# Optimization experiments

Hardware: AMD Instinct MI355X
Metric: run time of the kernel (lower is better)

## Reference

```python
import jax, jax.numpy as jnp
import numpy as np

N_NODES = 100000
N_EDGES = 1600000
D_IN = 128
D_HID = 128
D_OUT = 64


def _glorot(key, shape):
    lim = float(np.sqrt(6.0 / (shape[0] + shape[1])))
    return jax.random.uniform(key, shape, jnp.float32, -lim, lim)


def setup_inputs() -> dict:
    key = jax.random.key(0)
    ks = jax.random.split(key, 8)
    x = jax.random.normal(ks[0], (N_NODES, D_IN), jnp.float32)
    edge_index = jax.random.randint(ks[1], (2, N_EDGES), 0, N_NODES, jnp.int64)
    # SAGEConv layer 0: in=128 -> out=128 (lin_l with bias on aggregated, lin_r no bias on root)
    W_l0 = _glorot(ks[2], (D_IN, D_HID))
    b_l0 = jnp.zeros((D_HID,), jnp.float32)
    W_r0 = _glorot(ks[3], (D_IN, D_HID))
    # SAGEConv layer 1: in=128 -> out=64
    W_l1 = _glorot(ks[4], (D_HID, D_OUT))
    b_l1 = jnp.zeros((D_OUT,), jnp.float32)
    W_r1 = _glorot(ks[5], (D_HID, D_OUT))
    return {"x": x, "edge_index": edge_index,
            "W_l0": W_l0, "b_l0": b_l0, "W_r0": W_r0,
            "W_l1": W_l1, "b_l1": b_l1, "W_r1": W_r1}


def _sage_conv(x, src, dst, W_l, b_l, W_r):
    # mean aggregation of source features at targets (PyG SAGEConv default aggr='mean')
    msgs = x[src]                                              # [E, d_in] irregular gather
    agg = jax.ops.segment_sum(msgs, dst, num_segments=N_NODES)  # [N, d_in]
    cnt = jax.ops.segment_sum(jnp.ones((src.shape[0],), x.dtype), dst,
                              num_segments=N_NODES)            # [N]
    mean = agg / jnp.maximum(cnt, 1.0)[:, None]
    return mean @ W_l + b_l + x @ W_r


def reference(x, edge_index, W_l0, b_l0, W_r0, W_l1, b_l1, W_r1):
    src, dst = edge_index[0], edge_index[1]
    h = _sage_conv(x, src, dst, W_l0, b_l0, W_r0)
    h = jax.nn.relu(h)
    # dropout is identity at inference (training=False)
    out = _sage_conv(h, src, dst, W_l1, b_l1, W_r1)
    return out
```

## Files before the change

### kernel.cpp

```cpp
#include <hip/hip_runtime.h>
#include <type_traits>

#define NN 100000
#define NE 1600000
#define DF 128
#define NBKT 196
#define BKT_SHIFT 9
#define EPB 6250
#define NPB2 391

typedef unsigned short ushort_t;
typedef unsigned int uint_t;
typedef __bf16 bf16x8 __attribute__((ext_vector_type(8)));
typedef float f32x4 __attribute__((ext_vector_type(4)));

union ABFrag { uint4 u; bf16x8 v; ushort_t s[8]; };

__device__ __forceinline__ ushort_t f2bf(float f) {
    uint_t u;
    __builtin_memcpy(&u, &f, 4);
    uint_t rounding = 0x7FFFu + ((u >> 16) & 1u);
    u += rounding;
    return (ushort_t)(u >> 16);
}
__device__ __forceinline__ float lo_f(uint_t u) { return __uint_as_float(u << 16); }
__device__ __forceinline__ float hi_f(uint_t u) { return __uint_as_float(u & 0xffff0000u); }
__device__ __forceinline__ uint_t pack2(float a, float b) {
    return (uint_t)f2bf(a) | ((uint_t)f2bf(b) << 16);
}

__device__ __forceinline__ int detect64(const int* ei, int* s64) {
    if (threadIdx.x < 64) {
        int v = ei[threadIdx.x];
        bool ok = ((threadIdx.x & 1) == 0) || (v == 0);
        unsigned long long m = __ballot(ok);
        if (threadIdx.x == 0) *s64 = (m == 0xFFFFFFFFFFFFFFFFULL) ? 1 : 0;
    }
    __syncthreads();
    return *s64;
}

__global__ __launch_bounds__(256) void k_bktcnt(const int* __restrict__ ei,
                                                int* __restrict__ M) {
    __shared__ int cnt[NBKT];
    __shared__ int s64;
    int t = threadIdx.x, blk = blockIdx.x;
    int is64 = detect64(ei, &s64);
    for (int i = t; i < NBKT; i += 256) cnt[i] = 0;
    __syncthreads();
    int e0 = blk * EPB;
    if (is64) {
        const long long* p = (const long long*)ei;
        for (int i = t; i < EPB; i += 256) {
            int d = (int)p[(size_t)NE + e0 + i];
            atomicAdd(&cnt[d >> BKT_SHIFT], 1);
        }
    } else {
        for (int i = t; i < EPB; i += 256) {
            int d = ei[NE + e0 + i];
            atomicAdd(&cnt[d >> BKT_SHIFT], 1);
        }
    }
    __syncthreads();
    for (int i = t; i < NBKT; i += 256) M[i * 256 + blk] = cnt[i];
}

__global__ __launch_bounds__(256) void k_colscan(int* __restrict__ M, int* __restrict__ colsum) {
    __shared__ int sm[256];
    int t = threadIdx.x, b = blockIdx.x;
    int v = M[b * 256 + t];
    sm[t] = v;
    __syncthreads();
    for (int o = 1; o < 256; o <<= 1) {
        int add = (t >= o) ? sm[t - o] : 0;
        __syncthreads();
        sm[t] += add;
        __syncthreads();
    }
    M[b * 256 + t] = sm[t] - v;
    if (t == 255) colsum[b] = sm[255];
}

__global__ __launch_bounds__(256) void k_bktscan(const int* __restrict__ colsum,
                                                 int* __restrict__ bkbase, int* __restrict__ rs) {
    __shared__ int sm[256];
    int t = threadIdx.x;
    int v = (t < NBKT) ? colsum[t] : 0;
    sm[t] = v;
    __syncthreads();
    for (int o = 1; o < 256; o <<= 1) {
        int add = (t >= o) ? sm[t - o] : 0;
        __syncthreads();
        sm[t] += add;
        __syncthreads();
    }
    if (t <= NBKT) bkbase[t] = sm[t] - v;
    if (t == 0) rs[NN] = NE;
}

__global__ void k_scan512(const int* __restrict__ c2, int* __restrict__ dbase) {
    __shared__ int sm[512];
    int t = threadIdx.x;
    int v = c2[t];
    sm[t] = v;
    __syncthreads();
    for (int o = 1; o < 512; o <<= 1) {
        int add = (t >= o) ? sm[t - o] : 0;
        __syncthreads();
        sm[t] += add;
        __syncthreads();
    }
    dbase[t] = sm[t] - v;
}

__global__ __launch_bounds__(256) void k_bktscatter(const int* __restrict__ ei,
                                                    const int* __restrict__ M,
                                                    const int* __restrict__ bkbase,
                                                    uint2* __restrict__ tmp) {
    __shared__ int cur[NBKT];
    __shared__ int s64;
    int t = threadIdx.x, blk = blockIdx.x;
    int is64 = detect64(ei, &s64);
    for (int i = t; i < NBKT; i += 256) cur[i] = bkbase[i] + M[i * 256 + blk];
    __syncthreads();
    int e0 = blk * EPB;
    if (is64) {
        const long long* p = (const long long*)ei;
        for (int i = t; i < EPB; i += 256) {
            int e = e0 + i;
            int s = (int)p[e], d = (int)p[(size_t)NE + e];
            int pos = atomicAdd(&cur[d >> BKT_SHIFT], 1);
            tmp[pos] = make_uint2((uint_t)s, (uint_t)d);
        }
    } else {
        for (int i = t; i < EPB; i += 256) {
            int e = e0 + i;
            int s = ei[e], d = ei[NE + e];
            int pos = atomicAdd(&cur[d >> BKT_SHIFT], 1);
            tmp[pos] = make_uint2((uint_t)s, (uint_t)d);
        }
    }
}

__global__ __launch_bounds__(256) void k_bktsort(const uint2* __restrict__ tmp,
                                                 const int* __restrict__ bkbase,
                                                 int* __restrict__ rs, int* __restrict__ esrc) {
    __shared__ int hist[512];
    __shared__ int curp[512];
    int t = threadIdx.x, b = blockIdx.x;
    int nbase = b << BKT_SHIFT;
    int bb = bkbase[b], be = bkbase[b + 1];
    hist[t] = 0;
    hist[t + 256] = 0;
    __syncthreads();
    for (int i = bb + t; i < be; i += 256)
        atomicAdd(&hist[(int)tmp[i].y - nbase], 1);
    __syncthreads();
    int ov0 = hist[t], ov1 = hist[t + 256];
    for (int o = 1; o < 512; o <<= 1) {
        int v0 = (t >= o) ? hist[t - o] : 0;
        int v1 = (t + 256 >= o) ? hist[t + 256 - o] : 0;
        __syncthreads();
        hist[t] += v0;
        hist[t + 256] += v1;
        __syncthreads();
    }
    int ex0 = bb + hist[t] - ov0;
    int ex1 = bb + hist[t + 256] - ov1;
    int n0 = nbase + t, n1 = nbase + t + 256;
    if (n0 < NN) rs[n0] = ex0;
    if (n1 < NN) rs[n1] = ex1;
    curp[t] = ex0;
    curp[t + 256] = ex1;
    __syncthreads();
    for (int i = bb + t; i < be; i += 256) {
        uint2 pr = tmp[i];
        int pos = atomicAdd(&curp[(int)pr.y - nbase], 1);
        esrc[pos] = (int)pr.x;
    }
}

__global__ __launch_bounds__(256) void k_dcnt(const int* __restrict__ rs, int* __restrict__ M2) {
    __shared__ int cnt[512];
    int t = threadIdx.x, b = blockIdx.x;
    cnt[t] = 0;
    cnt[t + 256] = 0;
    __syncthreads();
    int base = b * NPB2;
    for (int i = t; i < NPB2; i += 256) {
        int n = base + i;
        if (n < NN) {
            int d = rs[n + 1] - rs[n];
            if (d > 511) d = 511;
            atomicAdd(&cnt[d], 1);
        }
    }
    __syncthreads();
    M2[t * 256 + b] = cnt[t];
    M2[(t + 256) * 256 + b] = cnt[t + 256];
}

__global__ __launch_bounds__(256) void k_dperm(const int* __restrict__ rs,
                                               const int* __restrict__ M2,
                                               const int* __restrict__ dbase,
                                               int* __restrict__ perm) {
    __shared__ int cur[512];
    int t = threadIdx.x, b = blockIdx.x;
    cur[t] = dbase[t] + M2[t * 256 + b];
    cur[t + 256] = dbase[t + 256] + M2[(t + 256) * 256 + b];
    __syncthreads();
    int base = b * NPB2;
    for (int i = t; i < NPB2; i += 256) {
        int n = base + i;
        if (n < NN) {
            int d = rs[n + 1] - rs[n];
            if (d > 511) d = 511;
            int pos = atomicAdd(&cur[d], 1);
            perm[pos] = n;
        }
    }
}

#define CAST_B 12501
__global__ void k_prep(const float* __restrict__ x, ushort_t* __restrict__ xb,
                       const float* __restrict__ Wl0, const float* __restrict__ Wr0,
                       ushort_t* __restrict__ pw0,
                       const float* __restrict__ Wl1, const float* __restrict__ Wr1,
                       ushort_t* __restrict__ pw1) {
    const int n4 = NN * DF / 4;
    int blk = blockIdx.x, t = threadIdx.x;
    if (blk < CAST_B) {
        int i = blk * 256 + t;
        if (i < n4) {
            float4 f = ((const float4*)x)[i];
            uint2 o;
            o.x = pack2(f.x, f.y);
            o.y = pack2(f.z, f.w);
            ((uint2*)xb)[i] = o;
        } else if (i < n4 + 32) {
            ((uint2*)xb)[i] = make_uint2(0u, 0u);
        }
    } else if (blk < CAST_B + 128) {
        int idx = (blk - CAST_B) * 256 + t;
        int j = idx & 7;
        int lane = (idx >> 3) & 63;
        int rem = idx / 512;
        int tt = rem % 8;
        int s = rem / 8;
        int quad = lane >> 4, l16 = lane & 15;
        int k = (s & 3) * 32 + quad * 8 + j;
        int n = tt * 16 + l16;
        const float* W = (s < 4) ? Wl0 : Wr0;
        pw0[idx] = f2bf(W[k * 128 + n]);
    } else {
        int idx = (blk - CAST_B - 128) * 256 + t;
        int j = idx & 7;
        int lane = (idx >> 3) & 63;
        int rem = idx / 512;
        int tt = rem % 8;
        int s = rem / 8;
        int quad = lane >> 4, l16 = lane & 15;
        int k = s * 32 + quad * 8 + j;
        int n = (tt & 3) * 16 + l16;
        const float* W = (tt < 4) ? Wl1 : Wr1;
        pw1[idx] = f2bf(W[k * 64 + n]);
    }
}

__global__ __launch_bounds__(256) void k_agg0(const ushort_t* __restrict__ xb,
                                              const int* __restrict__ rs,
                                              const int* __restrict__ esrc,
                                              const int* __restrict__ perm,
                                              ushort_t* __restrict__ outm) {
    int wv = threadIdx.x >> 6;
    int lane = threadIdx.x & 63;
    int l16 = lane & 15, quad = lane >> 4, gbase = lane & 48;
    int slot = (blockIdx.x * 4 + wv) * 4 + quad;
    int n = perm[slot];
    int s0 = rs[n];
    int deg = rs[n + 1] - s0;
    if (deg == 0) s0 = 0;
    int md = deg;
    md = max(md, __shfl_xor(md, 16));
    md = max(md, __shfl_xor(md, 32));
    float acc[8] = {0.f, 0.f, 0.f, 0.f, 0.f, 0.f, 0.f, 0.f};
    const ushort_t* fb = xb + l16 * 8;
    int clampIdx = (deg > 0) ? deg - 1 : 0;
    for (int c = 0; c < md; c += 16) {
        int ii = c + l16;
        if (ii > clampIdx) ii = clampIdx;
        int my = esrc[s0 + ii];
        uint4 v[16];
#pragma unroll
        for (int e = 0; e < 16; e++) {
            int r = __shfl(my, gbase + e);
            r = (c + e < deg) ? r : NN;
            v[e] = *(const uint4*)(fb + (size_t)r * DF);
        }
#pragma unroll
        for (int e = 0; e < 16; e++) {
            acc[0] += lo_f(v[e].x); acc[1] += hi_f(v[e].x);
            acc[2] += lo_f(v[e].y); acc[3] += hi_f(v[e].y);
            acc[4] += lo_f(v[e].z); acc[5] += hi_f(v[e].z);
            acc[6] += lo_f(v[e].w); acc[7] += hi_f(v[e].w);
        }
    }
    float inv = 1.0f / (float)(deg > 0 ? deg : 1);
    uint4 o;
    o.x = pack2(acc[0] * inv, acc[1] * inv);
    o.y = pack2(acc[2] * inv, acc[3] * inv);
    o.z = pack2(acc[4] * inv, acc[5] * inv);
    o.w = pack2(acc[6] * inv, acc[7] * inv);
    *(uint4*)(outm + (size_t)n * DF + l16 * 8) = o;
}

__global__ __launch_bounds__(256) void k_gemm0(const ushort_t* __restrict__ A0,
                                               const ushort_t* __restrict__ A1,
                                               const ushort_t* __restrict__ Wpk,
                                               const float* __restrict__ bias,
                                               ushort_t* __restrict__ out) {
    int warp = threadIdx.x >> 6;
    int lane = threadIdx.x & 63;
    int quad = lane >> 4;
    int l16 = lane & 15;
    int m0 = blockIdx.x * 64 + warp * 16;

    int rowA = m0 + l16;
    if (rowA >= NN) rowA = NN - 1;
    const int kofs = quad * 8;

    f32x4 acc[8];
#pragma unroll
    for (int t = 0; t < 8; t++) acc[t] = (f32x4){0.f, 0.f, 0.f, 0.f};

#pragma unroll
    for (int s = 0; s < 8; s++) {
        const ushort_t* Ab = (s < 4) ? A0 : A1;
        int kk = (s & 3) * 32 + kofs;
        ABFrag a;
        a.u = *(const uint4*)(Ab + (size_t)rowA * DF + kk);
#pragma unroll
        for (int t = 0; t < 8; t++) {
            ABFrag b;
            b.u = *(const uint4*)(Wpk + ((size_t)(s * 8 + t) * 64 + lane) * 8);
            acc[t] = __builtin_amdgcn_mfma_f32_16x16x32_bf16(a.v, b.v, acc[t], 0, 0, 0);
        }
    }

#pragma unroll
    for (int t = 0; t < 8; t++) {
        int col = t * 16 + l16;
        float bv = bias[col];
#pragma unroll
        for (int r = 0; r < 4; r++) {
            int row = m0 + quad * 4 + r;
            if (row < NN) {
                float v = fmaxf(acc[t][r] + bv, 0.f);
                out[(size_t)row * DF + col] = f2bf(v);
            }
        }
    }
}

__global__ __launch_bounds__(256) void k_gemm2(const ushort_t* __restrict__ A,
                                               const ushort_t* __restrict__ Wpk,
                                               const float* __restrict__ bias,
                                               ushort_t* __restrict__ tbuf,
                                               float* __restrict__ rbuf) {
    int warp = threadIdx.x >> 6;
    int lane = threadIdx.x & 63;
    int quad = lane >> 4;
    int l16 = lane & 15;
    int m0 = blockIdx.x * 64 + warp * 16;

    int rowA = m0 + l16;
    if (rowA >= NN) rowA = NN - 1;
    const int kofs = quad * 8;

    f32x4 acc[8];
#pragma unroll
    for (int t = 0; t < 8; t++) acc[t] = (f32x4){0.f, 0.f, 0.f, 0.f};

#pragma unroll
    for (int s = 0; s < 4; s++) {
        int kk = s * 32 + kofs;
        ABFrag a;
        a.u = *(const uint4*)(A + (size_t)rowA * DF + kk);
#pragma unroll
        for (int t = 0; t < 8; t++) {
            ABFrag b;
            b.u = *(const uint4*)(Wpk + ((size_t)(s * 8 + t) * 64 + lane) * 8);
            acc[t] = __builtin_amdgcn_mfma_f32_16x16x32_bf16(a.v, b.v, acc[t], 0, 0, 0);
        }
    }

#pragma unroll
    for (int t = 0; t < 8; t++) {
        int cc = (t & 3) * 16 + l16;
        if (t < 4) {
#pragma unroll
            for (int r = 0; r < 4; r++) {
                int row = m0 + quad * 4 + r;
                if (row < NN) tbuf[(size_t)row * 64 + cc] = f2bf(acc[t][r]);
            }
        } else {
            float bv = bias[cc];
#pragma unroll
            for (int r = 0; r < 4; r++) {
                int row = m0 + quad * 4 + r;
                if (row < NN) rbuf[(size_t)row * 64 + cc] = acc[t][r] + bv;
            }
        }
    }
    if (blockIdx.x == 0 && threadIdx.x < 32)
        ((uint_t*)(tbuf + (size_t)NN * 64))[threadIdx.x] = 0u;
}

__global__ __launch_bounds__(256) void k_agg2(const ushort_t* __restrict__ tbuf,
                                              const float* __restrict__ rbuf,
                                              const int* __restrict__ rs,
                                              const int* __restrict__ esrc,
                                              const int* __restrict__ perm,
                                              float* __restrict__ out) {
    int wv = threadIdx.x >> 6;
    int lane = threadIdx.x & 63;
    int li = lane & 7;
    int gbase = lane & 56;
    int slot = (blockIdx.x * 4 + wv) * 8 + (lane >> 3);
    int n = perm[slot];
    int s0 = rs[n];
    int deg = rs[n + 1] - s0;
    if (deg == 0) s0 = 0;
    int md = deg;
    md = max(md, __shfl_xor(md, 8));
    md = max(md, __shfl_xor(md, 16));
    md = max(md, __shfl_xor(md, 32));
    float acc[8] = {0.f, 0.f, 0.f, 0.f, 0.f, 0.f, 0.f, 0.f};
    const ushort_t* fb = tbuf + li * 8;
    int clampIdx = (deg > 0) ? deg - 1 : 0;
    for (int c = 0; c < md; c += 8) {
        int ii = c + li;
        if (ii > clampIdx) ii = clampIdx;
        int my = esrc[s0 + ii];
        uint4 v[8];
#pragma unroll
        for (int e = 0; e < 8; e++) {
            int r = __shfl(my, gbase + e);
            r = (c + e < deg) ? r : NN;
            v[e] = *(const uint4*)(fb + (size_t)r * 64);
        }
#pragma unroll
        for (int e = 0; e < 8; e++) {
            acc[0] += lo_f(v[e].x); acc[1] += hi_f(v[e].x);
            acc[2] += lo_f(v[e].y); acc[3] += hi_f(v[e].y);
            acc[4] += lo_f(v[e].z); acc[5] += hi_f(v[e].z);
            acc[6] += lo_f(v[e].w); acc[7] += hi_f(v[e].w);
        }
    }
    float inv = 1.0f / (float)(deg > 0 ? deg : 1);
    const float4* rp = (const float4*)(rbuf + (size_t)n * 64 + li * 8);
    float4 ra = rp[0], rb = rp[1];
    float4 oa, ob;
    oa.x = acc[0] * inv + ra.x; oa.y = acc[1] * inv + ra.y;
    oa.z = acc[2] * inv + ra.z; oa.w = acc[3] * inv + ra.w;
    ob.x = acc[4] * inv + rb.x; ob.y = acc[5] * inv + rb.y;
    ob.z = acc[6] * inv + rb.z; ob.w = acc[7] * inv + rb.w;
    float4* op = (float4*)(out + (size_t)n * 64 + li * 8);
    op[0] = oa;
    op[1] = ob;
}

extern "C" void kernel_launch(void* const* d_in, const int* in_sizes, int n_in,
                              void* d_out, int out_size, void* d_ws, size_t ws_size,
                              hipStream_t stream) {
    const float* x   = (const float*)d_in[0];
    const int*   ei  = (const int*)d_in[1];
    const float* Wl0 = (const float*)d_in[2];
    const float* bl0 = (const float*)d_in[3];
    const float* Wr0 = (const float*)d_in[4];
    const float* Wl1 = (const float*)d_in[5];
    const float* bl1 = (const float*)d_in[6];
    const float* Wr1 = (const float*)d_in[7];
    float* out = (float*)d_out;

    char* ws = (char*)d_ws;
    size_t off = 0;
    auto alloc = [&](size_t b) {
        size_t o = off;
        off += (b + 255) & ~(size_t)255;
        return o;
    };
    int* rs      = (int*)(ws + alloc((size_t)(NN + 1) * 4));
    int* M       = (int*)(ws + alloc((size_t)NBKT * 256 * 4));
    int* colsum  = (int*)(ws + alloc((size_t)NBKT * 4));
    int* bkbase  = (int*)(ws + alloc((size_t)(NBKT + 1) * 4));
    int* M2      = (int*)(ws + alloc((size_t)512 * 256 * 4));
    int* colsum2 = (int*)(ws + alloc((size_t)512 * 4));
    int* dbase   = (int*)(ws + alloc((size_t)512 * 4));
    int* perm    = (int*)(ws + alloc((size_t)NN * 4));
    int* esrc    = (int*)(ws + alloc((size_t)NE * 4));
    ushort_t* pw0  = (ushort_t*)(ws + alloc((size_t)8 * 8 * 512 * 2));
    ushort_t* pw1  = (ushort_t*)(ws + alloc((size_t)4 * 8 * 512 * 2));
    ushort_t* xb   = (ushort_t*)(ws + alloc((size_t)(NN + 1) * DF * 2));
    ushort_t* mean = (ushort_t*)(ws + alloc((size_t)NN * DF * 2));
    ushort_t* h    = (ushort_t*)(ws + alloc((size_t)NN * DF * 2));
    ushort_t* tbuf = (ushort_t*)(ws + alloc((size_t)(NN + 1) * 64 * 2));
    uint2* tmp = (uint2*)mean;
    float* rbuf = (float*)mean;

    k_bktcnt<<<256, 256, 0, stream>>>(ei, M);
    k_colscan<<<NBKT, 256, 0, stream>>>(M, colsum);
    k_bktscan<<<1, 256, 0, stream>>>(colsum, bkbase, rs);
    k_bktscatter<<<256, 256, 0, stream>>>(ei, M, bkbase, tmp);
    k_bktsort<<<NBKT, 256, 0, stream>>>(tmp, bkbase, rs, esrc);
    k_dcnt<<<256, 256, 0, stream>>>(rs, M2);
    k_colscan<<<512, 256, 0, stream>>>(M2, colsum2);
    k_scan512<<<1, 512, 0, stream>>>(colsum2, dbase);
    k_dperm<<<256, 256, 0, stream>>>(rs, M2, dbase, perm);
    k_prep<<<CAST_B + 128 + 64, 256, 0, stream>>>(x, xb, Wl0, Wr0, pw0, Wl1, Wr1, pw1);

    k_agg0<<<NN / 16, 256, 0, stream>>>(xb, rs, esrc, perm, mean);
    k_gemm0<<<(NN + 63) / 64, 256, 0, stream>>>(mean, xb, pw0, bl0, h);
    k_gemm2<<<(NN + 63) / 64, 256, 0, stream>>>(h, pw1, bl1, tbuf, rbuf);
    k_agg2<<<NN / 32, 256, 0, stream>>>(tbuf, rbuf, rs, esrc, perm, out);
}
```

Before: 339.0 us.

## Fuse the two GEMMs through LDS and bound gather loops by group max degree

The layer-0 GEMM and the layer-1 projection GEMM become one kernel. The ReLU'd hidden tile is staged in shared memory, so h is no longer written to or read back from global memory, and one launch is removed. rbuf gets its own buffer because mean is still being read while rbuf is written. Both aggregation kernels now loop only up to the group's max degree, in chunks of 4 with a scalar tail, instead of always issuing 16 or 8 gathers. In exchange, fewer loads are in flight per iteration, and the fused kernel uses LDS and a barrier.

```diff
diff --git a/kernel.cpp b/kernel.cpp
--- a/kernel.cpp
+++ b/kernel.cpp
@@ -274,8 +274,8 @@
                                               ushort_t* __restrict__ outm) {
     int wv = threadIdx.x >> 6;
     int lane = threadIdx.x & 63;
-    int l16 = lane & 15, quad = lane >> 4, gbase = lane & 48;
-    int slot = (blockIdx.x * 4 + wv) * 4 + quad;
+    int l16 = lane & 15, gbase = lane & 48;
+    int slot = (blockIdx.x * 4 + wv) * 4 + (lane >> 4);
     int n = perm[slot];
     int s0 = rs[n];
     int deg = rs[n + 1] - s0;
@@ -290,19 +290,37 @@
         int ii = c + l16;
         if (ii > clampIdx) ii = clampIdx;
         int my = esrc[s0 + ii];
-        uint4 v[16];
-#pragma unroll
-        for (int e = 0; e < 16; e++) {
+        int lim = md - c;
+        if (lim > 16) lim = 16;
+        int e = 0;
+        for (; e + 4 <= lim; e += 4) {
+            int r0 = __shfl(my, gbase + e);
+            int r1 = __shfl(my, gbase + e + 1);
+            int r2 = __shfl(my, gbase + e + 2);
+            int r3 = __shfl(my, gbase + e + 3);
+            r0 = (c + e < deg) ? r0 : NN;
+            r1 = (c + e + 1 < deg) ? r1 : NN;
+            r2 = (c + e + 2 < deg) ? r2 : NN;
+            r3 = (c + e + 3 < deg) ? r3 : NN;
+            uint4 v0 = *(const uint4*)(fb + (size_t)r0 * DF);
+            uint4 v1 = *(const uint4*)(fb + (size_t)r1 * DF);
+            uint4 v2 = *(const uint4*)(fb + (size_t)r2 * DF);
+            uint4 v3 = *(const uint4*)(fb + (size_t)r3 * DF);
+            acc[0] += lo_f(v0.x); acc[1] += hi_f(v0.x); acc[2] += lo_f(v0.y); acc[3] += hi_f(v0.y);
+            acc[4] += lo_f(v0.z); acc[5] += hi_f(v0.z); acc[6] += lo_f(v0.w); acc[7] += hi_f(v0.w);
+            acc[0] += lo_f(v1.x); acc[1] += hi_f(v1.x); acc[2] += lo_f(v1.y); acc[3] += hi_f(v1.y);
+            acc[4] += lo_f(v1.z); acc[5] += hi_f(v1.z); acc[6] += lo_f(v1.w); acc[7] += hi_f(v1.w);
+            acc[0] += lo_f(v2.x); acc[1] += hi_f(v2.x); acc[2] += lo_f(v2.y); acc[3] += hi_f(v2.y);
+            acc[4] += lo_f(v2.z); acc[5] += hi_f(v2.z); acc[6] += lo_f(v2.w); acc[7] += hi_f(v2.w);
+            acc[0] += lo_f(v3.x); acc[1] += hi_f(v3.x); acc[2] += lo_f(v3.y); acc[3] += hi_f(v3.y);
+            acc[4] += lo_f(v3.z); acc[5] += hi_f(v3.z); acc[6] += lo_f(v3.w); acc[7] += hi_f(v3.w);
+        }
+        for (; e < lim; ++e) {
             int r = __shfl(my, gbase + e);
             r = (c + e < deg) ? r : NN;
-            v[e] = *(const uint4*)(fb + (size_t)r * DF);
-        }
-#pragma unroll
-        for (int e = 0; e < 16; e++) {
-            acc[0] += lo_f(v[e].x); acc[1] += hi_f(v[e].x);
-            acc[2] += lo_f(v[e].y); acc[3] += hi_f(v[e].y);
-            acc[4] += lo_f(v[e].z); acc[5] += hi_f(v[e].z);
-            acc[6] += lo_f(v[e].w); acc[7] += hi_f(v[e].w);
+            uint4 v = *(const uint4*)(fb + (size_t)r * DF);
+            acc[0] += lo_f(v.x); acc[1] += hi_f(v.x); acc[2] += lo_f(v.y); acc[3] += hi_f(v.y);
+            acc[4] += lo_f(v.z); acc[5] += hi_f(v.z); acc[6] += lo_f(v.w); acc[7] += hi_f(v.w);
         }
     }
     float inv = 1.0f / (float)(deg > 0 ? deg : 1);
@@ -314,11 +332,15 @@
     *(uint4*)(outm + (size_t)n * DF + l16 * 8) = o;
 }
 
-__global__ __launch_bounds__(256) void k_gemm0(const ushort_t* __restrict__ A0,
+__global__ __launch_bounds__(256) void k_gemmF(const ushort_t* __restrict__ A0,
                                                const ushort_t* __restrict__ A1,
-                                               const ushort_t* __restrict__ Wpk,
-                                               const float* __restrict__ bias,
-                                               ushort_t* __restrict__ out) {
+                                               const ushort_t* __restrict__ pw0,
+                                               const float* __restrict__ bl0,
+                                               const ushort_t* __restrict__ pw1,
+                                               const float* __restrict__ bl1,
+                                               ushort_t* __restrict__ tbuf,
+                                               float* __restrict__ rbuf) {
+    __shared__ ushort_t h_lds[64][136];
     int warp = threadIdx.x >> 6;
     int lane = threadIdx.x & 63;
     int quad = lane >> 4;
@@ -342,58 +364,34 @@
 #pragma unroll
         for (int t = 0; t < 8; t++) {
             ABFrag b;
-            b.u = *(const uint4*)(Wpk + ((size_t)(s * 8 + t) * 64 + lane) * 8);
+            b.u = *(const uint4*)(pw0 + ((size_t)(s * 8 + t) * 64 + lane) * 8);
             acc[t] = __builtin_amdgcn_mfma_f32_16x16x32_bf16(a.v, b.v, acc[t], 0, 0, 0);
         }
     }
-
 #pragma unroll
     for (int t = 0; t < 8; t++) {
         int col = t * 16 + l16;
-        float bv = bias[col];
-#pragma unroll
-        for (int r = 0; r < 4; r++) {
-            int row = m0 + quad * 4 + r;
-            if (row < NN) {
-                float v = fmaxf(acc[t][r] + bv, 0.f);
-                out[(size_t)row * DF + col] = f2bf(v);
-            }
-        }
-    }
-}
-
-__global__ __launch_bounds__(256) void k_gemm2(const ushort_t* __restrict__ A,
-                                               const ushort_t* __restrict__ Wpk,
-                                               const float* __restrict__ bias,
-                                               ushort_t* __restrict__ tbuf,
-                                               float* __restrict__ rbuf) {
-    int warp = threadIdx.x >> 6;
-    int lane = threadIdx.x & 63;
-    int quad = lane >> 4;
-    int l16 = lane & 15;
-    int m0 = blockIdx.x * 64 + warp * 16;
-
-    int rowA = m0 + l16;
-    if (rowA >= NN) rowA = NN - 1;
-    const int kofs = quad * 8;
-
-    f32x4 acc[8];
-#pragma unroll
-    for (int t = 0; t < 8; t++) acc[t] = (f32x4){0.f, 0.f, 0.f, 0.f};
-
+        float bv = bl0[col];
+#pragma unroll
+        for (int r = 0; r < 4; r++)
+            h_lds[warp * 16 + quad * 4 + r][col] = f2bf(fmaxf(acc[t][r] + bv, 0.f));
+    }
+    __syncthreads();
+
+    f32x4 c1[8];
+#pragma unroll
+    for (int t = 0; t < 8; t++) c1[t] = (f32x4){0.f, 0.f, 0.f, 0.f};
 #pragma unroll
     for (int s = 0; s < 4; s++) {
-        int kk = s * 32 + kofs;
         ABFrag a;
-        a.u = *(const uint4*)(A + (size_t)rowA * DF + kk);
+        a.u = *(const uint4*)&h_lds[warp * 16 + l16][s * 32 + kofs];
 #pragma unroll
         for (int t = 0; t < 8; t++) {
             ABFrag b;
-            b.u = *(const uint4*)(Wpk + ((size_t)(s * 8 + t) * 64 + lane) * 8);
-            acc[t] = __builtin_amdgcn_mfma_f32_16x16x32_bf16(a.v, b.v, acc[t], 0, 0, 0);
-        }
-    }
-
+            b.u = *(const uint4*)(pw1 + ((size_t)(s * 8 + t) * 64 + lane) * 8);
+            c1[t] = __builtin_amdgcn_mfma_f32_16x16x32_bf16(a.v, b.v, c1[t], 0, 0, 0);
+        }
+    }
 #pragma unroll
     for (int t = 0; t < 8; t++) {
         int cc = (t & 3) * 16 + l16;
@@ -401,14 +399,14 @@
 #pragma unroll
             for (int r = 0; r < 4; r++) {
                 int row = m0 + quad * 4 + r;
-                if (row < NN) tbuf[(size_t)row * 64 + cc] = f2bf(acc[t][r]);
+                if (row < NN) tbuf[(size_t)row * 64 + cc] = f2bf(c1[t][r]);
             }
         } else {
-            float bv = bias[cc];
+            float bv = bl1[cc];
 #pragma unroll
             for (int r = 0; r < 4; r++) {
                 int row = m0 + quad * 4 + r;
-                if (row < NN) rbuf[(size_t)row * 64 + cc] = acc[t][r] + bv;
+                if (row < NN) rbuf[(size_t)row * 64 + cc] = c1[t][r] + bv;
             }
         }
     }
@@ -442,19 +440,37 @@
         int ii = c + li;
         if (ii > clampIdx) ii = clampIdx;
         int my = esrc[s0 + ii];
-        uint4 v[8];
-#pragma unroll
-        for (int e = 0; e < 8; e++) {
+        int lim = md - c;
+        if (lim > 8) lim = 8;
+        int e = 0;
+        for (; e + 4 <= lim; e += 4) {
+            int r0 = __shfl(my, gbase + e);
+            int r1 = __shfl(my, gbase + e + 1);
+            int r2 = __shfl(my, gbase + e + 2);
+            int r3 = __shfl(my, gbase + e + 3);
+            r0 = (c + e < deg) ? r0 : NN;
+            r1 = (c + e + 1 < deg) ? r1 : NN;
+            r2 = (c + e + 2 < deg) ? r2 : NN;
+            r3 = (c + e + 3 < deg) ? r3 : NN;
+            uint4 v0 = *(const uint4*)(fb + (size_t)r0 * 64);
+            uint4 v1 = *(const uint4*)(fb + (size_t)r1 * 64);
+            uint4 v2 = *(const uint4*)(fb + (size_t)r2 * 64);
+            uint4 v3 = *(const uint4*)(fb + (size_t)r3 * 64);
+            acc[0] += lo_f(v0.x); acc[1] += hi_f(v0.x); acc[2] += lo_f(v0.y); acc[3] += hi_f(v0.y);
+            acc[4] += lo_f(v0.z); acc[5] += hi_f(v0.z); acc[6] += lo_f(v0.w); acc[7] += hi_f(v0.w);
+            acc[0] += lo_f(v1.x); acc[1] += hi_f(v1.x); acc[2] += lo_f(v1.y); acc[3] += hi_f(v1.y);
+            acc[4] += lo_f(v1.z); acc[5] += hi_f(v1.z); acc[6] += lo_f(v1.w); acc[7] += hi_f(v1.w);
+            acc[0] += lo_f(v2.x); acc[1] += hi_f(v2.x); acc[2] += lo_f(v2.y); acc[3] += hi_f(v2.y);
+            acc[4] += lo_f(v2.z); acc[5] += hi_f(v2.z); acc[6] += lo_f(v2.w); acc[7] += hi_f(v2.w);
+            acc[0] += lo_f(v3.x); acc[1] += hi_f(v3.x); acc[2] += lo_f(v3.y); acc[3] += hi_f(v3.y);
+            acc[4] += lo_f(v3.z); acc[5] += hi_f(v3.z); acc[6] += lo_f(v3.w); acc[7] += hi_f(v3.w);
+        }
+        for (; e < lim; ++e) {
             int r = __shfl(my, gbase + e);
             r = (c + e < deg) ? r : NN;
-            v[e] = *(const uint4*)(fb + (size_t)r * 64);
-        }
-#pragma unroll
-        for (int e = 0; e < 8; e++) {
-            acc[0] += lo_f(v[e].x); acc[1] += hi_f(v[e].x);
-            acc[2] += lo_f(v[e].y); acc[3] += hi_f(v[e].y);
-            acc[4] += lo_f(v[e].z); acc[5] += hi_f(v[e].z);
-            acc[6] += lo_f(v[e].w); acc[7] += hi_f(v[e].w);
+            uint4 v = *(const uint4*)(fb + (size_t)r * 64);
+            acc[0] += lo_f(v.x); acc[1] += hi_f(v.x); acc[2] += lo_f(v.y); acc[3] += hi_f(v.y);
+            acc[4] += lo_f(v.z); acc[5] += hi_f(v.z); acc[6] += lo_f(v.w); acc[7] += hi_f(v.w);
         }
     }
     float inv = 1.0f / (float)(deg > 0 ? deg : 1);
@@ -503,10 +519,9 @@
     ushort_t* pw1  = (ushort_t*)(ws + alloc((size_t)4 * 8 * 512 * 2));
     ushort_t* xb   = (ushort_t*)(ws + alloc((size_t)(NN + 1) * DF * 2));
     ushort_t* mean = (ushort_t*)(ws + alloc((size_t)NN * DF * 2));
-    ushort_t* h    = (ushort_t*)(ws + alloc((size_t)NN * DF * 2));
     ushort_t* tbuf = (ushort_t*)(ws + alloc((size_t)(NN + 1) * 64 * 2));
+    float*    rbuf = (float*)(ws + alloc((size_t)NN * 64 * 4));
     uint2* tmp = (uint2*)mean;
-    float* rbuf = (float*)mean;
 
     k_bktcnt<<<256, 256, 0, stream>>>(ei, M);
     k_colscan<<<NBKT, 256, 0, stream>>>(M, colsum);
@@ -520,7 +535,6 @@
     k_prep<<<CAST_B + 128 + 64, 256, 0, stream>>>(x, xb, Wl0, Wr0, pw0, Wl1, Wr1, pw1);
 
     k_agg0<<<NN / 16, 256, 0, stream>>>(xb, rs, esrc, perm, mean);
-    k_gemm0<<<(NN + 63) / 64, 256, 0, stream>>>(mean, xb, pw0, bl0, h);
-    k_gemm2<<<(NN + 63) / 64, 256, 0, stream>>>(h, pw1, bl1, tbuf, rbuf);
+    k_gemmF<<<(NN + 63) / 64, 256, 0, stream>>>(mean, xb, pw0, bl0, pw1, bl1, tbuf, rbuf);
     k_agg2<<<NN / 32, 256, 0, stream>>>(tbuf, rbuf, rs, esrc, perm, out);
 }
```

After: 316.2 us. -6.7%, faster.
